# Kernel tuning notes

Measured on AMD Instinct MI355X. Metric: run time of the kernel, lower is better.

## Reference

```python
import jax, jax.numpy as jnp
import numpy as np

NUM_EMBEDDINGS = 1024
EMBEDDING_DIM = 64
COMMITMENT_COST = 0.25


def setup_inputs() -> dict:
    key = jax.random.key(0)
    k1, k2 = jax.random.split(key)
    latents = jax.random.normal(k1, (64, EMBEDDING_DIM, 32, 32), dtype=jnp.float32)
    # torch init: uniform_(-1/num_embeddings, 1/num_embeddings)
    codebook = jax.random.uniform(
        k2, (NUM_EMBEDDINGS, EMBEDDING_DIM), dtype=jnp.float32,
        minval=-1.0 / NUM_EMBEDDINGS, maxval=1.0 / NUM_EMBEDDINGS)
    return {"latents": latents, "codebook": codebook}


def reference(latents, codebook):
    B, C, H, W = latents.shape
    K = codebook.shape[0]
    x = jnp.transpose(latents, (0, 2, 3, 1))            # [B,H,W,C]
    x_flat = x.reshape(-1, C)                            # [N,C]
    # squared euclidean distances [N,K]
    dist = (jnp.sum(x_flat ** 2, axis=1, keepdims=True)
            + jnp.sum(codebook ** 2, axis=1)
            - 2.0 * x_flat @ codebook.T)
    idx = jnp.argmin(dist, axis=1)                       # [N] int
    q_flat = codebook[idx]                               # [N,C]
    q = q_flat.reshape(x.shape)                          # [B,H,W,C]
    e_loss = jnp.mean((jax.lax.stop_gradient(q) - x) ** 2)
    q_loss = jnp.mean((q - jax.lax.stop_gradient(x)) ** 2)
    vq_loss = q_loss + COMMITMENT_COST * e_loss
    # straight-through estimator
    q_st = x + jax.lax.stop_gradient(q - x)
    quantized = jnp.transpose(q_st, (0, 3, 1, 2))        # [B,C,H,W]
    # perplexity from code usage histogram
    N = x_flat.shape[0]
    avg_probs = jnp.zeros((K,), dtype=jnp.float32).at[idx].add(1.0) / N
    perplexity = jnp.exp(-jnp.sum(avg_probs * jnp.log(avg_probs + 1e-10)))
    encoding_indices = idx.reshape(B, H, W)
    return (vq_loss, quantized, perplexity, encoding_indices)
```

## Files before the change

kernel.cpp:

```cpp
#include <hip/hip_runtime.h>

#define N_PTS   65536
#define K_CODES 1024
#define C_DIM   64
#define HW      1024
#define Q_ELEMS 4194304

#define OUT_Q_OFF 1
#define OUT_P_OFF 4194305
#define OUT_I_OFF 4194306

#define WS_HIST 0
#define WS_SSE  4096
#define WS_CSUM 8192
#define WS_CBP  16384

#define EPS_A_W 7.5e-5f
#define EPS_T_W 2.0e-4f

typedef float f32x16 __attribute__((ext_vector_type(16)));
typedef short bf16x8 __attribute__((ext_vector_type(8)));

__device__ __forceinline__ unsigned short bf16rn(float f) {
    unsigned int u = __float_as_uint(f);
    return (unsigned short)((u + 0x7FFFu + ((u >> 16) & 1u)) >> 16);
}
__device__ __forceinline__ float bf16tof(unsigned short h) {
    return __uint_as_float(((unsigned int)h) << 16);
}

__device__ __forceinline__ float np_pairwise_sumsq64(const float* a) {
    float r[8];
    #pragma unroll
    for (int j = 0; j < 8; ++j) r[j] = __fmul_rn(a[j], a[j]);
    #pragma unroll
    for (int i = 8; i < 64; i += 8) {
        #pragma unroll
        for (int j = 0; j < 8; ++j)
            r[j] = __fadd_rn(r[j], __fmul_rn(a[i + j], a[i + j]));
    }
    return __fadd_rn(__fadd_rn(__fadd_rn(r[0], r[1]), __fadd_rn(r[2], r[3])),
                     __fadd_rn(__fadd_rn(r[4], r[5]), __fadd_rn(r[6], r[7])));
}

__global__ void vq_prep(const float* __restrict__ cb, float* __restrict__ csum,
                        unsigned short* __restrict__ cbp,
                        unsigned int* __restrict__ hist,
                        double* __restrict__ sse) {
    int g = blockIdx.x * 256 + threadIdx.x;
    if (g < 1024) hist[g] = 0u;
    if (g == 1024) *sse = 0.0;
    int t = g >> 6, lane = g & 63, l31 = lane & 31, half = lane >> 5;
    int row = t * 32 + l31;
    const float* r = cb + row * 64;
    float cs = np_pairwise_sumsq64(r);
    if (half == 0) csum[row] = cs;
    size_t tb = (size_t)t * 9 * 512;
    #pragma unroll
    for (int c = 0; c < 4; ++c) {
        bf16x8 h8, l8;
        #pragma unroll
        for (int j = 0; j < 8; ++j) {
            float f = r[c * 16 + half * 8 + j];
            unsigned short h = bf16rn(f);
            h8[j] = (short)h;
            l8[j] = (short)bf16rn(f - bf16tof(h));
        }
        *(bf16x8*)(cbp + tb + (size_t)(c * 2 + 0) * 512 + lane * 8) = h8;
        *(bf16x8*)(cbp + tb + (size_t)(c * 2 + 1) * 512 + lane * 8) = l8;
    }
    bf16x8 c8;
    #pragma unroll
    for (int j = 0; j < 8; ++j) c8[j] = 0;
    if (half == 0) c8[0] = (short)bf16rn(-0.5f * cs);
    *(bf16x8*)(cbp + tb + (size_t)8 * 512 + lane * 8) = c8;
}

__global__ __launch_bounds__(512, 2) void vq_main(
        const float* __restrict__ latents,
        const float* __restrict__ cb,
        const float* __restrict__ csum,
        const unsigned short* __restrict__ cbp,
        unsigned int* __restrict__ hist,
        double* __restrict__ sse,
        float* __restrict__ out) {
    __shared__ float xs[128 * 65];
    __shared__ float tmax[32 * 128];
    __shared__ float m1s[8 * 32], m2s[8 * 32];
    __shared__ int   i1s[8 * 32];
    __shared__ float m1f[128];
    __shared__ int   fk[128], ambig[128], acount;
    __shared__ double wred[8];

    const int tid  = threadIdx.x;
    const int lane = tid & 63, wave = tid >> 6;
    const int grp = wave >> 1, thalf = wave & 1;
    const int n0 = blockIdx.x * 128;
    const int b = n0 >> 10, hw0 = n0 & 1023;
    const float* xg = latents + (size_t)b * C_DIM * HW + hw0;

    for (int i = tid; i < 128 * 64; i += 512) {
        int p = i & 127, d = i >> 7;
        xs[p * 65 + d] = xg[(size_t)d * HW + p];
    }
    if (tid == 0) acount = 0;
    __syncthreads();

    const int l31 = lane & 31, half = lane >> 5;
    const int pb = (grp << 5) + l31;
    bf16x8 xh[4], xl[4], x4;
    #pragma unroll
    for (int c = 0; c < 4; ++c)
        #pragma unroll
        for (int j = 0; j < 8; ++j) {
            float f = xs[pb * 65 + c * 16 + half * 8 + j];
            unsigned short h = bf16rn(f);
            xh[c][j] = (short)h;
            xl[c][j] = (short)bf16rn(f - bf16tof(h));
        }
    #pragma unroll
    for (int j = 0; j < 8; ++j) x4[j] = 0;
    if (half == 0) x4[0] = (short)0x3F80;

    f32x16 zacc;
    #pragma unroll
    for (int r = 0; r < 16; ++r) zacc[r] = 0.0f;

    float m1 = -3e38f, m2 = -3e38f;
    int i1 = 0;
    const int RC[16] = {0,1,2,3,8,9,10,11,16,17,18,19,24,25,26,27};
    const int rh4 = half * 4;
    const bf16x8* base = (const bf16x8*)cbp;

    auto load_tile = [&](int t, bf16x8* ch, bf16x8* cl, bf16x8& ca) {
        const bf16x8* bp = base + (size_t)t * 576 + lane;
        #pragma unroll
        for (int c = 0; c < 4; ++c) {
            ch[c] = bp[c * 128];
            cl[c] = bp[c * 128 + 64];
        }
        ca = bp[512];
    };
    auto screen_tile = [&](int t, const bf16x8* ch, const bf16x8* cl, bf16x8 ca) {
        f32x16 acc = __builtin_amdgcn_mfma_f32_32x32x16_bf16(ca, x4, zacc, 0, 0, 0);
        #pragma unroll
        for (int c = 0; c < 4; ++c)
            acc = __builtin_amdgcn_mfma_f32_32x32x16_bf16(ch[c], xh[c], acc, 0, 0, 0);
        #pragma unroll
        for (int c = 0; c < 4; ++c)
            acc = __builtin_amdgcn_mfma_f32_32x32x16_bf16(ch[c], xl[c], acc, 0, 0, 0);
        #pragma unroll
        for (int c = 0; c < 4; ++c)
            acc = __builtin_amdgcn_mfma_f32_32x32x16_bf16(cl[c], xh[c], acc, 0, 0, 0);
        float vl = -3e38f, sl = -3e38f;
        int kl = 0;
        #pragma unroll
        for (int r = 0; r < 16; ++r) {
            float v = acc[r];
            sl = __builtin_amdgcn_fmed3f(v, sl, vl);
            bool c2 = v > vl;
            kl = c2 ? RC[r] : kl;
            vl = fmaxf(vl, v);
        }
        int k = (t << 5) + rh4 + kl;
        bool cg = vl > m1;
        i1 = cg ? k : i1;
        float X = cg ? sl : m2;
        m2 = __builtin_amdgcn_fmed3f(vl, X, m1);
        m1 = fmaxf(m1, vl);
        float tlm = fmaxf(vl, __shfl_xor(vl, 32, 64));
        if (half == 0) tmax[t * 128 + pb] = tlm;
    };

    bf16x8 chA[4], clA[4], caA, chB[4], clB[4], caB;
    const int t0 = thalf << 4;
    load_tile(t0, chA, clA, caA);
    for (int t = t0; t < t0 + 16; t += 2) {
        load_tile(t + 1, chB, clB, caB);
        screen_tile(t, chA, clA, caA);
        if (t + 2 < t0 + 16) load_tile(t + 2, chA, clA, caA);
        screen_tile(t + 1, chB, clB, caB);
    }
    {
        float m1o = __shfl_xor(m1, 32, 64);
        float m2o = __shfl_xor(m2, 32, 64);
        int   i1o = __shfl_xor(i1, 32, 64);
        m2 = fmaxf(fmaxf(m2, m2o), fminf(m1, m1o));
        i1 = (m1o > m1) ? i1o : i1;
        m1 = fmaxf(m1, m1o);
        if (half == 0) {
            m1s[wave * 32 + l31] = m1;
            m2s[wave * 32 + l31] = m2;
            i1s[wave * 32 + l31] = i1;
        }
    }
    __syncthreads();
    if (tid < 128) {
        int p = tid, l = p & 31, wA = (p >> 5) * 2;
        float a1 = m1s[wA * 32 + l], a2 = m2s[wA * 32 + l];
        float b1 = m1s[wA * 32 + 32 + l], b2 = m2s[wA * 32 + 32 + l];
        int   ai = i1s[wA * 32 + l],  bi = i1s[wA * 32 + 32 + l];
        bool cg = b1 > a1;
        float mm1 = fmaxf(a1, b1);
        float mm2 = __builtin_amdgcn_fmed3f(a1, b1, cg ? b2 : a2);
        m1f[p] = mm1;
        fk[p]  = cg ? bi : ai;
        if (mm2 >= mm1 - EPS_A_W) {
            int a = atomicAdd(&acount, 1);
            ambig[a] = p;
        }
    }
    __syncthreads();

    for (int a = wave; a < acount; a += 8) {
        int p = ambig[a];
        const float* xrow = &xs[p * 65];
        float Aq = np_pairwise_sumsq64(xrow);
        float thr = m1f[p] - EPS_T_W;
        unsigned long long best = ~0ULL;
        for (int t = 0; t < 32; ++t) {
            if (tmax[t * 128 + p] < thr) continue;
            if (lane < 32) {
                int k = (t << 5) + lane;
                const float* crow = cb + (size_t)k * 64;
                float m = 0.0f;
                #pragma unroll
                for (int d = 0; d < 64; ++d) m = __fmaf_rn(xrow[d], crow[d], m);
                float D = __fsub_rn(__fadd_rn(Aq, csum[k]), __fmul_rn(2.0f, m));
                unsigned long long key =
                    ((unsigned long long)__float_as_uint(D) << 10) | (unsigned)k;
                best = (key < best) ? key : best;
            }
        }
        #pragma unroll
        for (int off = 32; off > 0; off >>= 1) {
            unsigned long long o = __shfl_xor(best, off, 64);
            best = (o < best) ? o : best;
        }
        if (lane == 0) fk[p] = (int)(best & 1023ULL);
    }
    __syncthreads();

    if (tid < 128) {
        int myk = fk[tid];
        out[OUT_I_OFF + n0 + tid] = (float)myk;
        atomicAdd(&hist[myk], 1u);
    }
    double e = 0.0;
    #pragma unroll
    for (int i2 = 0; i2 < 4; ++i2) {
        int i = tid + i2 * 512;
        int p = i >> 4, seg = i & 15;
        const float4 q = *(const float4*)(cb + (size_t)fk[p] * 64 + seg * 4);
        float* xp = &xs[p * 65 + seg * 4];
        float x0 = xp[0], x1 = xp[1], x2 = xp[2], x3 = xp[3];
        double d0 = (double)x0 - (double)q.x; e = fma(d0, d0, e);
        double d1 = (double)x1 - (double)q.y; e = fma(d1, d1, e);
        double d2 = (double)x2 - (double)q.z; e = fma(d2, d2, e);
        double d3 = (double)x3 - (double)q.w; e = fma(d3, d3, e);
        xp[0] = q.x; xp[1] = q.y; xp[2] = q.z; xp[3] = q.w;
    }
    #pragma unroll
    for (int off = 32; off > 0; off >>= 1) e += __shfl_down(e, off, 64);
    if (lane == 0) wred[wave] = e;
    __syncthreads();
    if (tid == 0) {
        double s = 0.0;
        #pragma unroll
        for (int w = 0; w < 8; ++w) s += wred[w];
        atomicAdd(sse, s);
    }
    for (int i = tid; i < 128 * 64; i += 512) {
        int p = i & 127, c = i >> 7;
        out[OUT_Q_OFF + (size_t)b * 65536 + (size_t)c * HW + hw0 + p] = xs[p * 65 + c];
    }
}

__global__ void vq_final(const unsigned int* __restrict__ hist,
                         const double* __restrict__ sse,
                         float* __restrict__ out) {
    __shared__ double red[256];
    int t = threadIdx.x;
    double s = 0.0;
    for (int i = t; i < K_CODES; i += 256) {
        double p = (double)hist[i] / (double)N_PTS;
        s += p * log(p + 1e-10);
    }
    red[t] = s;
    __syncthreads();
    for (int w = 128; w > 0; w >>= 1) {
        if (t < w) red[t] += red[t + w];
        __syncthreads();
    }
    if (t == 0) {
        out[OUT_P_OFF] = (float)exp(-red[0]);
        out[0] = (float)(1.25 * sse[0] / (double)Q_ELEMS);
    }
}

extern "C" void kernel_launch(void* const* d_in, const int* in_sizes, int n_in,
                              void* d_out, int out_size, void* d_ws, size_t ws_size,
                              hipStream_t stream) {
    const float* latents = (const float*)d_in[0];
    const float* cb      = (const float*)d_in[1];
    float* out = (float*)d_out;
    char* ws = (char*)d_ws;

    unsigned int*   hist = (unsigned int*)(ws + WS_HIST);
    double*         sse  = (double*)(ws + WS_SSE);
    float*          csum = (float*)(ws + WS_CSUM);
    unsigned short* cbp  = (unsigned short*)(ws + WS_CBP);

    vq_prep <<<8, 256, 0, stream>>>(cb, csum, cbp, hist, sse);
    vq_main <<<N_PTS / 128, 512, 0, stream>>>(latents, cb, csum, cbp,
                                              hist, sse, out);
    vq_final<<<1, 256, 0, stream>>>(hist, sse, out);
}
```

Before: 136.3 us.

## Stage codebook tiles in LDS via async global_load_lds with block-wide double buffer

```diff
diff --git a/kernel.cpp b/kernel.cpp
--- a/kernel.cpp
+++ b/kernel.cpp
@@ -27,6 +27,12 @@
 }
 __device__ __forceinline__ float bf16tof(unsigned short h) {
     return __uint_as_float(((unsigned int)h) << 16);
+}
+
+__device__ __forceinline__ void gload_lds16(const void* g, void* l) {
+    __builtin_amdgcn_global_load_lds(
+        (const __attribute__((address_space(1))) unsigned int*)g,
+        (__attribute__((address_space(3))) unsigned int*)l, 16, 0, 0);
 }
 
 __device__ __forceinline__ float np_pairwise_sumsq64(const float* a) {
@@ -55,7 +61,7 @@
     const float* r = cb + row * 64;
     float cs = np_pairwise_sumsq64(r);
     if (half == 0) csum[row] = cs;
-    size_t tb = (size_t)t * 9 * 512;
+    size_t tb = (size_t)t * 4096;
     #pragma unroll
     for (int c = 0; c < 4; ++c) {
         bf16x8 h8, l8;
@@ -69,14 +75,9 @@
         *(bf16x8*)(cbp + tb + (size_t)(c * 2 + 0) * 512 + lane * 8) = h8;
         *(bf16x8*)(cbp + tb + (size_t)(c * 2 + 1) * 512 + lane * 8) = l8;
     }
-    bf16x8 c8;
-    #pragma unroll
-    for (int j = 0; j < 8; ++j) c8[j] = 0;
-    if (half == 0) c8[0] = (short)bf16rn(-0.5f * cs);
-    *(bf16x8*)(cbp + tb + (size_t)8 * 512 + lane * 8) = c8;
-}
-
-__global__ __launch_bounds__(512, 2) void vq_main(
+}
+
+__global__ __launch_bounds__(256, 1) void vq_main(
         const float* __restrict__ latents,
         const float* __restrict__ cb,
         const float* __restrict__ csum,
@@ -86,29 +87,29 @@
         float* __restrict__ out) {
     __shared__ float xs[128 * 65];
     __shared__ float tmax[32 * 128];
-    __shared__ float m1s[8 * 32], m2s[8 * 32];
-    __shared__ int   i1s[8 * 32];
+    __shared__ float csl[1024];
+    __shared__ __align__(16) short stg[2][2048];
     __shared__ float m1f[128];
     __shared__ int   fk[128], ambig[128], acount;
-    __shared__ double wred[8];
+    __shared__ double wred[4];
 
     const int tid  = threadIdx.x;
     const int lane = tid & 63, wave = tid >> 6;
-    const int grp = wave >> 1, thalf = wave & 1;
     const int n0 = blockIdx.x * 128;
     const int b = n0 >> 10, hw0 = n0 & 1023;
     const float* xg = latents + (size_t)b * C_DIM * HW + hw0;
 
-    for (int i = tid; i < 128 * 64; i += 512) {
+    for (int i = tid; i < 128 * 64; i += 256) {
         int p = i & 127, d = i >> 7;
         xs[p * 65 + d] = xg[(size_t)d * HW + p];
     }
+    for (int i = tid; i < 1024; i += 256) csl[i] = -0.5f * csum[i];
     if (tid == 0) acount = 0;
     __syncthreads();
 
     const int l31 = lane & 31, half = lane >> 5;
-    const int pb = (grp << 5) + l31;
-    bf16x8 xh[4], xl[4], x4;
+    const int pb = (wave << 5) + l31;
+    bf16x8 xh[4], xl[4];
     #pragma unroll
     for (int c = 0; c < 4; ++c)
         #pragma unroll
@@ -118,9 +119,6 @@
             xh[c][j] = (short)h;
             xl[c][j] = (short)bf16rn(f - bf16tof(h));
         }
-    #pragma unroll
-    for (int j = 0; j < 8; ++j) x4[j] = 0;
-    if (half == 0) x4[0] = (short)0x3F80;
 
     f32x16 zacc;
     #pragma unroll
@@ -130,33 +128,51 @@
     int i1 = 0;
     const int RC[16] = {0,1,2,3,8,9,10,11,16,17,18,19,24,25,26,27};
     const int rh4 = half * 4;
-    const bf16x8* base = (const bf16x8*)cbp;
-
-    auto load_tile = [&](int t, bf16x8* ch, bf16x8* cl, bf16x8& ca) {
-        const bf16x8* bp = base + (size_t)t * 576 + lane;
-        #pragma unroll
-        for (int c = 0; c < 4; ++c) {
-            ch[c] = bp[c * 128];
-            cl[c] = bp[c * 128 + 64];
-        }
-        ca = bp[512];
-    };
-    auto screen_tile = [&](int t, const bf16x8* ch, const bf16x8* cl, bf16x8 ca) {
-        f32x16 acc = __builtin_amdgcn_mfma_f32_32x32x16_bf16(ca, x4, zacc, 0, 0, 0);
-        #pragma unroll
-        for (int c = 0; c < 4; ++c)
-            acc = __builtin_amdgcn_mfma_f32_32x32x16_bf16(ch[c], xh[c], acc, 0, 0, 0);
-        #pragma unroll
-        for (int c = 0; c < 4; ++c)
-            acc = __builtin_amdgcn_mfma_f32_32x32x16_bf16(ch[c], xl[c], acc, 0, 0, 0);
-        #pragma unroll
-        for (int c = 0; c < 4; ++c)
-            acc = __builtin_amdgcn_mfma_f32_32x32x16_bf16(cl[c], xh[c], acc, 0, 0, 0);
+    const char* cbpB = (const char*)cbp;
+    char* lds0 = (char*)&stg[0][0] + wave * 1024;
+    char* lds1 = (char*)&stg[1][0] + wave * 1024;
+
+    gload_lds16(cbpB + (size_t)tid * 16, lds0);
+
+    for (int t = 0; t < 32; ++t) {
+        __syncthreads();
+        const bf16x8* s0 = (const bf16x8*)&stg[0][0];
+        bf16x8 a0 = s0[lane], a1 = s0[64 + lane], a2 = s0[128 + lane], a3 = s0[192 + lane];
+        f32x16 csv;
+        {
+            const int cb0 = (t << 5) + rh4;
+            #pragma unroll
+            for (int q = 0; q < 4; ++q) {
+                float4 c4 = *(const float4*)&csl[cb0 + q * 8];
+                csv[q * 4 + 0] = c4.x; csv[q * 4 + 1] = c4.y;
+                csv[q * 4 + 2] = c4.z; csv[q * 4 + 3] = c4.w;
+            }
+        }
+        gload_lds16(cbpB + ((size_t)(2 * t + 1)) * 4096 + (size_t)tid * 16, lds1);
+        f32x16 acc0 = __builtin_amdgcn_mfma_f32_32x32x16_bf16(a0, xh[0], csv, 0, 0, 0);
+        acc0 = __builtin_amdgcn_mfma_f32_32x32x16_bf16(a0, xl[0], acc0, 0, 0, 0);
+        acc0 = __builtin_amdgcn_mfma_f32_32x32x16_bf16(a1, xh[0], acc0, 0, 0, 0);
+        acc0 = __builtin_amdgcn_mfma_f32_32x32x16_bf16(a2, xh[1], acc0, 0, 0, 0);
+        acc0 = __builtin_amdgcn_mfma_f32_32x32x16_bf16(a2, xl[1], acc0, 0, 0, 0);
+        acc0 = __builtin_amdgcn_mfma_f32_32x32x16_bf16(a3, xh[1], acc0, 0, 0, 0);
+
+        __syncthreads();
+        const bf16x8* s1 = (const bf16x8*)&stg[1][0];
+        bf16x8 b0 = s1[lane], b1 = s1[64 + lane], b2 = s1[128 + lane], b3 = s1[192 + lane];
+        if (t < 31)
+            gload_lds16(cbpB + ((size_t)(2 * t + 2)) * 4096 + (size_t)tid * 16, lds0);
+        f32x16 acc1 = __builtin_amdgcn_mfma_f32_32x32x16_bf16(b0, xh[2], zacc, 0, 0, 0);
+        acc1 = __builtin_amdgcn_mfma_f32_32x32x16_bf16(b0, xl[2], acc1, 0, 0, 0);
+        acc1 = __builtin_amdgcn_mfma_f32_32x32x16_bf16(b1, xh[2], acc1, 0, 0, 0);
+        acc1 = __builtin_amdgcn_mfma_f32_32x32x16_bf16(b2, xh[3], acc1, 0, 0, 0);
+        acc1 = __builtin_amdgcn_mfma_f32_32x32x16_bf16(b2, xl[3], acc1, 0, 0, 0);
+        acc1 = __builtin_amdgcn_mfma_f32_32x32x16_bf16(b3, xh[3], acc1, 0, 0, 0);
+
         float vl = -3e38f, sl = -3e38f;
         int kl = 0;
         #pragma unroll
         for (int r = 0; r < 16; ++r) {
-            float v = acc[r];
+            float v = acc0[r] + acc1[r];
             sl = __builtin_amdgcn_fmed3f(v, sl, vl);
             bool c2 = v > vl;
             kl = c2 ? RC[r] : kl;
@@ -170,17 +186,8 @@
         m1 = fmaxf(m1, vl);
         float tlm = fmaxf(vl, __shfl_xor(vl, 32, 64));
         if (half == 0) tmax[t * 128 + pb] = tlm;
-    };
-
-    bf16x8 chA[4], clA[4], caA, chB[4], clB[4], caB;
-    const int t0 = thalf << 4;
-    load_tile(t0, chA, clA, caA);
-    for (int t = t0; t < t0 + 16; t += 2) {
-        load_tile(t + 1, chB, clB, caB);
-        screen_tile(t, chA, clA, caA);
-        if (t + 2 < t0 + 16) load_tile(t + 2, chA, clA, caA);
-        screen_tile(t + 1, chB, clB, caB);
-    }
+    }
+
     {
         float m1o = __shfl_xor(m1, 32, 64);
         float m2o = __shfl_xor(m2, 32, 64);
@@ -189,30 +196,17 @@
         i1 = (m1o > m1) ? i1o : i1;
         m1 = fmaxf(m1, m1o);
         if (half == 0) {
-            m1s[wave * 32 + l31] = m1;
-            m2s[wave * 32 + l31] = m2;
-            i1s[wave * 32 + l31] = i1;
-        }
-    }
-    __syncthreads();
-    if (tid < 128) {
-        int p = tid, l = p & 31, wA = (p >> 5) * 2;
-        float a1 = m1s[wA * 32 + l], a2 = m2s[wA * 32 + l];
-        float b1 = m1s[wA * 32 + 32 + l], b2 = m2s[wA * 32 + 32 + l];
-        int   ai = i1s[wA * 32 + l],  bi = i1s[wA * 32 + 32 + l];
-        bool cg = b1 > a1;
-        float mm1 = fmaxf(a1, b1);
-        float mm2 = __builtin_amdgcn_fmed3f(a1, b1, cg ? b2 : a2);
-        m1f[p] = mm1;
-        fk[p]  = cg ? bi : ai;
-        if (mm2 >= mm1 - EPS_A_W) {
-            int a = atomicAdd(&acount, 1);
-            ambig[a] = p;
-        }
-    }
-    __syncthreads();
-
-    for (int a = wave; a < acount; a += 8) {
+            m1f[pb] = m1;
+            fk[pb] = i1;
+            if (m2 >= m1 - EPS_A_W) {
+                int a = atomicAdd(&acount, 1);
+                ambig[a] = pb;
+            }
+        }
+    }
+    __syncthreads();
+
+    for (int a = wave; a < acount; a += 4) {
         int p = ambig[a];
         const float* xrow = &xs[p * 65];
         float Aq = np_pairwise_sumsq64(xrow);
@@ -248,8 +242,8 @@
     }
     double e = 0.0;
     #pragma unroll
-    for (int i2 = 0; i2 < 4; ++i2) {
-        int i = tid + i2 * 512;
+    for (int i2 = 0; i2 < 8; ++i2) {
+        int i = tid + i2 * 256;
         int p = i >> 4, seg = i & 15;
         const float4 q = *(const float4*)(cb + (size_t)fk[p] * 64 + seg * 4);
         float* xp = &xs[p * 65 + seg * 4];
@@ -267,10 +261,10 @@
     if (tid == 0) {
         double s = 0.0;
         #pragma unroll
-        for (int w = 0; w < 8; ++w) s += wred[w];
+        for (int w = 0; w < 4; ++w) s += wred[w];
         atomicAdd(sse, s);
     }
-    for (int i = tid; i < 128 * 64; i += 512) {
+    for (int i = tid; i < 128 * 64; i += 256) {
         int p = i & 127, c = i >> 7;
         out[OUT_Q_OFF + (size_t)b * 65536 + (size_t)c * HW + hw0 + p] = xs[p * 65 + c];
     }
@@ -312,7 +306,7 @@
     unsigned short* cbp  = (unsigned short*)(ws + WS_CBP);
 
     vq_prep <<<8, 256, 0, stream>>>(cb, csum, cbp, hist, sse);
-    vq_main <<<N_PTS / 128, 512, 0, stream>>>(latents, cb, csum, cbp,
+    vq_main <<<N_PTS / 128, 256, 0, stream>>>(latents, cb, csum, cbp,
                                               hist, sse, out);
     vq_final<<<1, 256, 0, stream>>>(hist, sse, out);
 }
```

After: 136.8 us. About the same (+0.4%).
